# Kernel tuning notes

Measured on AMD Instinct MI355X. Metric: run time of the kernel, lower is better.

## Reference

```python
import jax, jax.numpy as jnp
import numpy as np

BN_EPS = 1e-5


def setup_inputs() -> dict:
    key = jax.random.key(0)
    ks = jax.random.split(key, 4)
    B, C, H, W = 4, 256, 64, 64
    Ck, Cv = 64, 256
    x = jax.random.normal(ks[0], (B, C, H, W), dtype=jnp.float32)
    Wk = jax.random.normal(ks[1], (Ck, C), dtype=jnp.float32) * (1.0 / np.sqrt(C))
    bk = jax.random.normal(ks[2], (Ck,), dtype=jnp.float32) * 0.02
    Wv = jax.random.normal(ks[3], (Cv, C), dtype=jnp.float32) * (1.0 / np.sqrt(C))
    bv = jnp.zeros((Cv,), dtype=jnp.float32)
    return {
        "x": x,
        "Wk": Wk,
        "bk": bk,
        "bn_gamma": jnp.ones((Ck,), dtype=jnp.float32),
        "bn_beta": jnp.zeros((Ck,), dtype=jnp.float32),
        "bn_mean": jnp.zeros((Ck,), dtype=jnp.float32),
        "bn_var": jnp.ones((Ck,), dtype=jnp.float32),
        "Wv": Wv,
        "bv": bv,
    }


def reference(x, Wk, bk, bn_gamma, bn_beta, bn_mean, bn_var, Wv, bv):
    B, C, H, W = x.shape
    HW = H * W
    # 1x1 conv == channel matmul; f_query = f_key (shared weights), so Q == K
    k = jnp.einsum("bchw,kc->bkhw", x, Wk) + bk[None, :, None, None]
    # BatchNorm2d (inference mode: running stats)
    inv = bn_gamma * jax.lax.rsqrt(bn_var + BN_EPS)
    k = k * inv[None, :, None, None] + (bn_beta - bn_mean * inv)[None, :, None, None]
    k = k.reshape(B, -1, HW)                      # [B, Ck, HW]
    v = (jnp.einsum("bchw,kc->bkhw", x, Wv) + bv[None, :, None, None]).reshape(B, -1, HW)  # [B, Cv, HW]
    # energy[b,i,j] = sum_c Q[b,c,i] * K[b,c,j]  (no scaling, as in source)
    energy = jnp.einsum("bci,bcj->bij", k, k)     # [B, HW, HW]
    attn = jax.nn.softmax(energy, axis=-1)
    # out[b,c,i] = sum_j V[b,c,j] * attn[i,j]
    out = jnp.einsum("bcj,bij->bci", v, attn)
    return out.reshape(B, -1, H, W)
```

## Files before the change

### kernel.cpp

```cpp
#include <hip/hip_runtime.h>
#include <math.h>

#define BN_EPS 1e-5f

constexpr int B  = 4;
constexpr int C  = 256;
constexpr int HW = 4096;
constexpr int CK = 64;
constexpr int CV = 256;
constexpr int CO = 320;
constexpr int CHG = 2;

typedef short bf16x8 __attribute__((ext_vector_type(8)));
typedef float f32x4  __attribute__((ext_vector_type(4)));
typedef unsigned uint32x4 __attribute__((ext_vector_type(4)));

__device__ __forceinline__ ushort f2bf(float f) {
    unsigned u = __float_as_uint(f);
    u += 0x7FFFu + ((u >> 16) & 1u);
    return (ushort)(u >> 16);
}

__device__ __forceinline__ unsigned cvtpk_bf16(float lo, float hi) {
    unsigned r;
    asm("v_cvt_pk_bf16_f32 %0, %1, %2" : "=v"(r) : "v"(lo), "v"(hi));
    return r;
}

__device__ __forceinline__ int swzk(int r) {
    return (((r & 3) | ((((r >> 2) ^ (r >> 3)) & 1) << 2)) << 4);
}
__device__ __forceinline__ int swzv(int r) { return (r & 7) << 4; }

__device__ __forceinline__ void gload_lds16(const void* g, void* l) {
    __builtin_amdgcn_global_load_lds(
        (const __attribute__((address_space(1))) unsigned*)g,
        (__attribute__((address_space(3))) unsigned*)l, 16, 0, 0);
}

__global__ __launch_bounds__(256) void wprep(
    const float* __restrict__ Wk, const float* __restrict__ bk,
    const float* __restrict__ gamma, const float* __restrict__ beta,
    const float* __restrict__ mean,  const float* __restrict__ var,
    const float* __restrict__ Wv, const float* __restrict__ bv,
    ushort* __restrict__ Wq, float* __restrict__ bq, unsigned* __restrict__ Mx)
{
    const int co = blockIdx.x;
    const int c  = threadIdx.x;
    if (co < B && c == 0) Mx[co] = 0u;
    float w;
    if (co < CK) {
        float inv = gamma[co] * rsqrtf(var[co] + BN_EPS);
        w = Wk[co * C + c] * inv;
        if (c == 0) bq[co] = bk[co] * inv + (beta[co] - mean[co] * inv);
    } else {
        w = Wv[(co - CK) * C + c];
        if (c == 0) bq[co] = bv[co - CK];
    }
    const int wv  = co / 80, rem = co % 80;
    const int mi  = rem / 16, colw = rem % 16;
    const int ks  = c >> 5, qw = (c >> 3) & 3, e = c & 7;
    Wq[((((((wv * 8 + ks) * 5 + mi) * 4 + qw) * 16 + colw)) << 3) + e] = f2bf(w);
}

__global__ __launch_bounds__(256) void kv_gemm(
    const float* __restrict__ x, const ushort* __restrict__ Wq,
    const float* __restrict__ bq,
    ushort* __restrict__ Kbuf, ushort* __restrict__ Vbuf,
    float* __restrict__ mb, unsigned* __restrict__ Mx)
{
    __shared__ __align__(16) ushort xt[32][C + 8];

    const int t    = threadIdx.x;
    const int lane = t & 63;
    const int wv   = t >> 6;
    const int q    = lane >> 4;
    const int col  = lane & 15;
    const int hw0  = blockIdx.x * 32;
    const int b    = blockIdx.y;

    const float* xb = x + (size_t)b * C * HW;

    {
        const int cq  = (t >> 5) * 4;
        const int hwo = t & 31;
#pragma unroll
        for (int pass = 0; pass < 8; pass++) {
            const int c0 = pass * 32;
            float a0 = xb[(size_t)(c0 + cq + 0) * HW + hw0 + hwo];
            float a1 = xb[(size_t)(c0 + cq + 1) * HW + hw0 + hwo];
            float a2 = xb[(size_t)(c0 + cq + 2) * HW + hw0 + hwo];
            float a3 = xb[(size_t)(c0 + cq + 3) * HW + hw0 + hwo];
            ushort4 u = make_ushort4(f2bf(a0), f2bf(a1), f2bf(a2), f2bf(a3));
            *(ushort4*)&xt[hwo][c0 + cq] = u;
        }
    }
    __syncthreads();

    f32x4 acc[5][2];
#pragma unroll
    for (int mi = 0; mi < 5; mi++)
#pragma unroll
        for (int nt = 0; nt < 2; nt++)
            acc[mi][nt] = (f32x4){0.f, 0.f, 0.f, 0.f};

#pragma unroll
    for (int ks = 0; ks < 8; ks++) {
        bf16x8 av[5], bvv[2];
#pragma unroll
        for (int mi = 0; mi < 5; mi++)
            av[mi] = *(const bf16x8*)(Wq + ((size_t)((wv * 8 + ks) * 5 + mi) << 9) + lane * 8);
#pragma unroll
        for (int nt = 0; nt < 2; nt++)
            bvv[nt] = *(const bf16x8*)&xt[nt * 16 + col][ks * 32 + q * 8];
#pragma unroll
        for (int mi = 0; mi < 5; mi++)
#pragma unroll
            for (int nt = 0; nt < 2; nt++)
                acc[mi][nt] = __builtin_amdgcn_mfma_f32_16x16x32_bf16(bvv[nt], av[mi], acc[mi][nt], 0, 0, 0);
    }

    float ssq[2][4] = {{0.f,0.f,0.f,0.f},{0.f,0.f,0.f,0.f}};
#pragma unroll
    for (int mi = 0; mi < 5; mi++) {
        const int cot = wv * 80 + mi * 16;
        const float bi = bq[cot + col];
#pragma unroll
        for (int nt = 0; nt < 2; nt++) {
            const int hwr = hw0 + nt * 16 + q * 4;
            float v0 = acc[mi][nt][0] + bi;
            float v1 = acc[mi][nt][1] + bi;
            float v2 = acc[mi][nt][2] + bi;
            float v3 = acc[mi][nt][3] + bi;
            if (cot < CK) {
                const int ck = cot + col;
                Kbuf[((size_t)b * HW + hwr + 0) * CK + ck] = f2bf(v0);
                Kbuf[((size_t)b * HW + hwr + 1) * CK + ck] = f2bf(v1);
                Kbuf[((size_t)b * HW + hwr + 2) * CK + ck] = f2bf(v2);
                Kbuf[((size_t)b * HW + hwr + 3) * CK + ck] = f2bf(v3);
                ssq[nt][0] += v0 * v0; ssq[nt][1] += v1 * v1;
                ssq[nt][2] += v2 * v2; ssq[nt][3] += v3 * v3;
            } else {
                const int cv = cot - CK + col;
                ushort4 vv = make_ushort4(f2bf(v0), f2bf(v1), f2bf(v2), f2bf(v3));
                *(ushort4*)&Vbuf[((size_t)b * CV + cv) * HW + hwr] = vv;
            }
        }
    }

    if (wv == 0) {
        float mxn = 0.f;
#pragma unroll
        for (int nt = 0; nt < 2; nt++) {
#pragma unroll
            for (int off = 1; off <= 8; off <<= 1)
#pragma unroll
                for (int r = 0; r < 4; r++)
                    ssq[nt][r] += __shfl_xor(ssq[nt][r], off, 64);
            float4 nr = make_float4(sqrtf(ssq[nt][0]), sqrtf(ssq[nt][1]),
                                    sqrtf(ssq[nt][2]), sqrtf(ssq[nt][3]));
            if (col == 0)
                *(float4*)&mb[(size_t)b * HW + hw0 + nt * 16 + q * 4] = nr;
            mxn = fmaxf(mxn, fmaxf(fmaxf(nr.x, nr.y), fmaxf(nr.z, nr.w)));
        }
#pragma unroll
        for (int off = 1; off <= 32; off <<= 1)
            mxn = fmaxf(mxn, __shfl_xor(mxn, off, 64));
        if (t == 0) atomicMax(Mx + b, __float_as_uint(mxn));
    }
}

__global__ __launch_bounds__(256, 2) void attn_kernel(
    const ushort* __restrict__ Kbuf, const ushort* __restrict__ Vbuf,
    const float* __restrict__ mb, const unsigned* __restrict__ Mx,
    float* __restrict__ out)
{
    __shared__ __align__(16) ushort Kt[2][64 * 64];
    __shared__ __align__(16) ushort Vt[2][128 * 64];

    const int t    = threadIdx.x;
    const int lane = t & 63;
    const int wv   = t >> 6;
    const int q    = lane >> 4;
    const int col  = lane & 15;

    const unsigned lin = blockIdx.x + 64u * (blockIdx.y + (unsigned)CHG * blockIdx.z);
    const int xcd   = lin & 7;
    const int s_    = lin >> 3;
    const int i0g   = s_ * 64;
    const int chg   = xcd & 1;
    const int b     = xcd >> 1;

    const int iw    = wv * 16 + col;
    const int jperm = (col >> 2) * 8 + (col & 3);

    const ushort* Kb = Kbuf + (size_t)b * HW * CK;
    const ushort* Vb = Vbuf + (size_t)b * CV * HW;
    const int cbase = chg * 128;

    bf16x8 qa[2];
#pragma unroll
    for (int k = 0; k < 2; k++)
        qa[k] = *(const bf16x8*)(Kb + (size_t)(i0g + iw) * CK + k * 32 + q * 8);

    const float Mxf = __uint_as_float(Mx[b]);
    const float m_val = mb[(size_t)b * HW + i0g + iw] * Mxf;

    f32x4 Oacc[8];
#pragma unroll
    for (int mt = 0; mt < 8; mt++)
        Oacc[mt] = (f32x4){0.f, 0.f, 0.f, 0.f};

    float l_acc = 0.f;
    const f32x4 zf = (f32x4){0.f, 0.f, 0.f, 0.f};

#define STAGE(BUF, JN)                                                         \
    {                                                                          \
        const int jn_s = (JN);                                                 \
        _Pragma("unroll")                                                      \
        for (int p = 0; p < 2; p++) {                                          \
            int off = (wv * 2 + p) * 1024 + lane * 16;                         \
            int r = off >> 7, cb = off & 127;                                  \
            const char* g = (const char*)Kb + (size_t)(jn_s + r) * 128         \
                            + (cb ^ swzk(r));                                  \
            gload_lds16(g, (char*)&Kt[BUF][0] + off);                          \
        }                                                                      \
        _Pragma("unroll")                                                      \
        for (int p = 0; p < 4; p++) {                                          \
            int off = (wv * 4 + p) * 1024 + lane * 16;                         \
            int r = off >> 7, cb = off & 127;                                  \
            const char* g = (const char*)Vb                                    \
                            + ((size_t)(cbase + r) * HW + jn_s) * 2            \
                            + (cb ^ swzv(r));                                  \
            gload_lds16(g, (char*)&Vt[BUF][0] + off);                          \
        }                                                                      \
    }

    STAGE(0, 0);
    __syncthreads();

    int cur = 0;
    for (int j0 = 0; j0 < HW; j0 += 64) {
        STAGE(cur ^ 1, (j0 + 64) & (HW - 1));

        const char* KtB = (const char*)&Kt[cur][0];
        const char* VtB = (const char*)&Vt[cur][0];

        f32x4 S[4];
        __builtin_amdgcn_s_setprio(1);
#pragma unroll
        for (int nt = 0; nt < 4; nt++) {
            const int jr = jperm + (nt >> 1) * 32 + (nt & 1) * 4;
            bf16x8 k0 = *(const bf16x8*)(KtB + jr * 128 + ((q * 16) ^ swzk(jr)));
            bf16x8 k1 = *(const bf16x8*)(KtB + jr * 128 + ((64 + q * 16) ^ swzk(jr)));
            S[nt] = __builtin_amdgcn_mfma_f32_16x16x32_bf16(k0, qa[0], zf, 0, 0, 0);
            S[nt] = __builtin_amdgcn_mfma_f32_16x16x32_bf16(k1, qa[1], S[nt], 0, 0, 0);
        }
        __builtin_amdgcn_s_setprio(0);

        float p[4][4];
#pragma unroll
        for (int nt = 0; nt < 4; nt++) {
            p[nt][0] = __expf(S[nt][0] - m_val);
            p[nt][1] = __expf(S[nt][1] - m_val);
            p[nt][2] = __expf(S[nt][2] - m_val);
            p[nt][3] = __expf(S[nt][3] - m_val);
            l_acc += (p[nt][0] + p[nt][1]) + (p[nt][2] + p[nt][3]);
        }
        uint32x4 U0, U1;
        U0[0] = cvtpk_bf16(p[0][0], p[0][1]);
        U0[1] = cvtpk_bf16(p[0][2], p[0][3]);
        U0[2] = cvtpk_bf16(p[1][0], p[1][1]);
        U0[3] = cvtpk_bf16(p[1][2], p[1][3]);
        U1[0] = cvtpk_bf16(p[2][0], p[2][1]);
        U1[1] = cvtpk_bf16(p[2][2], p[2][3]);
        U1[2] = cvtpk_bf16(p[3][0], p[3][1]);
        U1[3] = cvtpk_bf16(p[3][2], p[3][3]);
        bf16x8 w0 = __builtin_bit_cast(bf16x8, U0);
        bf16x8 w1 = __builtin_bit_cast(bf16x8, U1);

        __builtin_amdgcn_s_setprio(1);
#pragma unroll
        for (int mt = 0; mt < 8; mt++) {
            const int vr = mt * 16 + col;
            bf16x8 v0 = *(const bf16x8*)(VtB + vr * 128 + ((q * 16) ^ swzv(vr)));
            bf16x8 v1 = *(const bf16x8*)(VtB + vr * 128 + ((64 + q * 16) ^ swzv(vr)));
            Oacc[mt] = __builtin_amdgcn_mfma_f32_16x16x32_bf16(v0, w0, Oacc[mt], 0, 0, 0);
            Oacc[mt] = __builtin_amdgcn_mfma_f32_16x16x32_bf16(v1, w1, Oacc[mt], 0, 0, 0);
        }
        __builtin_amdgcn_s_setprio(0);

        __syncthreads();
        cur ^= 1;
    }
#undef STAGE

    l_acc += __shfl_xor(l_acc, 16, 64);
    l_acc += __shfl_xor(l_acc, 32, 64);
    const float inv = 1.0f / l_acc;

    float* ob = out + (size_t)b * CV * HW;
#pragma unroll
    for (int mt = 0; mt < 8; mt++)
#pragma unroll
        for (int r = 0; r < 4; r++)
            ob[(size_t)(cbase + mt * 16 + q * 4 + r) * HW + i0g + iw] = Oacc[mt][r] * inv;
}

extern "C" void kernel_launch(void* const* d_in, const int* in_sizes, int n_in,
                              void* d_out, int out_size, void* d_ws, size_t ws_size,
                              hipStream_t stream)
{
    const float* x     = (const float*)d_in[0];
    const float* Wk    = (const float*)d_in[1];
    const float* bk    = (const float*)d_in[2];
    const float* gamma = (const float*)d_in[3];
    const float* beta  = (const float*)d_in[4];
    const float* mean  = (const float*)d_in[5];
    const float* var   = (const float*)d_in[6];
    const float* Wv    = (const float*)d_in[7];
    const float* bv    = (const float*)d_in[8];
    float* out = (float*)d_out;

    ushort*   Kbuf = (ushort*)d_ws;
    ushort*   Vbuf = Kbuf + (size_t)B * HW * CK;
    ushort*   Wq   = Vbuf + (size_t)B * CV * HW;
    float*    bq   = (float*)(Wq + (size_t)CO * C);
    float*    mb   = bq + CO;
    unsigned* Mx   = (unsigned*)(mb + (size_t)B * HW);

    wprep<<<dim3(CO), 256, 0, stream>>>(Wk, bk, gamma, beta, mean, var, Wv, bv, Wq, bq, Mx);

    kv_gemm<<<dim3(HW / 32, B), 256, 0, stream>>>(x, Wq, bq, Kbuf, Vbuf, mb, Mx);

    dim3 g2(HW / 64, CHG, B);
    attn_kernel<<<g2, 256, 0, stream>>>(Kbuf, Vbuf, mb, Mx, out);
}
```

Measured before the change: 171.6 us.

## Split attention key dimension across two blocks with atomic accumulation

Splits the key/value sequence loop of the attention kernel into two halves handled by separate blocks, doubling the grid. Partial outputs and softmax denominators are accumulated with float atomicAdd into a zeroed output and a new L buffer, and a new normalization kernel divides afterwards. This relies on the fixed max-norm bound so partials share one reference max. The aim is more parallelism and occupancy; the cost is two memsets, many global float atomics, an extra pass over the output, and nondeterministic summation order.

Result: slower. 197.1 us (+14.9%).

```diff
diff --git a/kernel.cpp b/kernel.cpp
--- a/kernel.cpp
+++ b/kernel.cpp
@@ -10,6 +10,7 @@
 constexpr int CV = 256;
 constexpr int CO = 320;
 constexpr int CHG = 2;
+constexpr int JS  = 2;
 
 typedef short bf16x8 __attribute__((ext_vector_type(8)));
 typedef float f32x4  __attribute__((ext_vector_type(4)));
@@ -173,7 +174,7 @@
 __global__ __launch_bounds__(256, 2) void attn_kernel(
     const ushort* __restrict__ Kbuf, const ushort* __restrict__ Vbuf,
     const float* __restrict__ mb, const unsigned* __restrict__ Mx,
-    float* __restrict__ out)
+    float* __restrict__ out, float* __restrict__ Lbuf)
 {
     __shared__ __align__(16) ushort Kt[2][64 * 64];
     __shared__ __align__(16) ushort Vt[2][128 * 64];
@@ -184,13 +185,16 @@
     const int q    = lane >> 4;
     const int col  = lane & 15;
 
-    const unsigned lin = blockIdx.x + 64u * (blockIdx.y + (unsigned)CHG * blockIdx.z);
+    const unsigned lin = blockIdx.x + 64u * (blockIdx.y + 4u * blockIdx.z);
     const int xcd   = lin & 7;
     const int s_    = lin >> 3;
-    const int i0g   = s_ * 64;
-    const int chg   = xcd & 1;
-    const int b     = xcd >> 1;
-
+    const int combo = xcd + 8 * (s_ >> 6);
+    const int i0g   = (s_ & 63) * 64;
+    const int chg   = combo & 1;
+    const int js    = (combo >> 1) & 1;
+    const int b     = combo >> 2;
+
+    const int jbase = js * (HW / JS);
     const int iw    = wv * 16 + col;
     const int jperm = (col >> 2) * 8 + (col & 3);
 
@@ -236,12 +240,12 @@
         }                                                                      \
     }
 
-    STAGE(0, 0);
+    STAGE(0, jbase);
     __syncthreads();
 
     int cur = 0;
-    for (int j0 = 0; j0 < HW; j0 += 64) {
-        STAGE(cur ^ 1, (j0 + 64) & (HW - 1));
+    for (int jo = 0; jo < HW / JS; jo += 64) {
+        STAGE(cur ^ 1, jbase + ((jo + 64) & (HW / JS - 1)));
 
         const char* KtB = (const char*)&Kt[cur][0];
         const char* VtB = (const char*)&Vt[cur][0];
@@ -297,14 +301,29 @@
 
     l_acc += __shfl_xor(l_acc, 16, 64);
     l_acc += __shfl_xor(l_acc, 32, 64);
-    const float inv = 1.0f / l_acc;
+    if (chg == 0 && q == 0)
+        atomicAdd(Lbuf + (size_t)b * HW + i0g + iw, l_acc);
 
     float* ob = out + (size_t)b * CV * HW;
 #pragma unroll
     for (int mt = 0; mt < 8; mt++)
 #pragma unroll
         for (int r = 0; r < 4; r++)
-            ob[(size_t)(cbase + mt * 16 + q * 4 + r) * HW + i0g + iw] = Oacc[mt][r] * inv;
+            atomicAdd(&ob[(size_t)(cbase + mt * 16 + q * 4 + r) * HW + i0g + iw],
+                      Oacc[mt][r]);
+}
+
+__global__ __launch_bounds__(256) void norm_out(
+    float* __restrict__ out, const float* __restrict__ Lbuf)
+{
+    const int g    = blockIdx.x * 256 + threadIdx.x;
+    const int flat = g * 4;
+    const int i    = flat & (HW - 1);
+    const int b    = flat >> 20;
+    float4 o = *(float4*)&out[flat];
+    const float4 l4 = *(const float4*)&Lbuf[(size_t)b * HW + i];
+    o.x /= l4.x; o.y /= l4.y; o.z /= l4.z; o.w /= l4.w;
+    *(float4*)&out[flat] = o;
 }
 
 extern "C" void kernel_launch(void* const* d_in, const int* in_sizes, int n_in,
@@ -327,12 +346,18 @@
     ushort*   Wq   = Vbuf + (size_t)B * CV * HW;
     float*    bq   = (float*)(Wq + (size_t)CO * C);
     float*    mb   = bq + CO;
-    unsigned* Mx   = (unsigned*)(mb + (size_t)B * HW);
+    float*    Lbuf = mb + (size_t)B * HW;
+    unsigned* Mx   = (unsigned*)(Lbuf + (size_t)B * HW);
+
+    hipMemsetAsync(Lbuf, 0, (size_t)B * HW * sizeof(float), stream);
+    hipMemsetAsync(out, 0, (size_t)out_size * sizeof(float), stream);
 
     wprep<<<dim3(CO), 256, 0, stream>>>(Wk, bk, gamma, beta, mean, var, Wv, bv, Wq, bq, Mx);
 
     kv_gemm<<<dim3(HW / 32, B), 256, 0, stream>>>(x, Wq, bq, Kbuf, Vbuf, mb, Mx);
 
-    dim3 g2(HW / 64, CHG, B);
-    attn_kernel<<<g2, 256, 0, stream>>>(Kbuf, Vbuf, mb, Mx, out);
-}
+    dim3 g2(HW / 64, CHG * JS, B);
+    attn_kernel<<<g2, 256, 0, stream>>>(Kbuf, Vbuf, mb, Mx, out, Lbuf);
+
+    norm_out<<<dim3(out_size / 4 / 256), 256, 0, stream>>>(out, Lbuf);
+}
```
